# Performance work log

Measured on AMD Instinct MI355X. Metric: run time of the kernel, lower is better.

Reference implementation:

```python
import jax, jax.numpy as jnp
import numpy as np


def setup_inputs() -> dict:
    key = jax.random.key(0)
    k1, k2, k3, k4 = jax.random.split(key, 4)
    N_NODES, N_RELS, N_TRIPLES, H = 100000, 100000, 300000, 256
    node_states = jax.random.normal(k1, (N_NODES, H), dtype=jnp.float32)
    rel_states = jax.random.normal(k2, (N_RELS, H), dtype=jnp.float32)
    triples = jax.random.randint(k3, (N_TRIPLES, 3), 0, N_NODES, dtype=jnp.int64)
    # nn.Linear(2H, H): weight (H, 2H) in torch; store transposed (2H, H) for x @ W
    W = jax.random.normal(k4, (2 * H, H), dtype=jnp.float32) * (1.0 / np.sqrt(2 * H))
    b = jnp.zeros((H,), dtype=jnp.float32)
    return {"node_states": node_states, "rel_states": rel_states, "triples": triples, "W": W, "b": b}


def reference(node_states, rel_states, triples, W, b):
    # triples columns: (subj_idx, rel_idx, obj_idx)
    subj_idx, rel_idx, obj_idx = triples[:, 0], triples[:, 1], triples[:, 2]
    rel = rel_states[rel_idx]                              # (T, H)
    msg_s2o = node_states[subj_idx] + rel                  # (T, H)
    msg_o2s = node_states[obj_idx] + rel                   # (T, H)
    agg = jnp.zeros_like(node_states)
    agg = agg.at[obj_idx].add(msg_s2o)
    agg = agg.at[subj_idx].add(msg_o2s)
    h = jnp.concatenate([node_states, agg], axis=-1)       # (N, 2H)
    h = h @ W + b                                          # (N, H)
    h = jax.nn.silu(h)
    return node_states + h
```

## Files before the change

### kernel.cpp

```cpp
#include <hip/hip_runtime.h>

#define H 256
typedef unsigned int  uint;
typedef unsigned short ushort;
typedef float  floatx4 __attribute__((ext_vector_type(4)));
typedef short  shortx8 __attribute__((ext_vector_type(8)));

__device__ __forceinline__ ushort bf16rn(float f) {
    uint u = __float_as_uint(f);
    u += 0x7FFF + ((u >> 16) & 1);
    return (ushort)(u >> 16);
}
__device__ __forceinline__ uint pkbf2(float a, float b) {
    return (uint)bf16rn(a) | ((uint)bf16rn(b) << 16);
}
__device__ __forceinline__ void atomic_pk_bf16(void* addr, uint v) {
    asm volatile("global_atomic_pk_add_bf16 %0, %1, off" :: "v"(addr), "v"(v) : "memory");
}
__device__ __forceinline__ void glds16(const void* g, void* l) {
    __builtin_amdgcn_global_load_lds(
        (__attribute__((address_space(1))) void*)(unsigned long long)(g),
        (__attribute__((address_space(3))) void*)(l), 16, 0, 0);
}

__global__ __launch_bounds__(256) void wt_kernel(const float* __restrict__ W,
                                                 ushort* __restrict__ Wt) {
    int k = blockIdx.x;
    int n = threadIdx.x;
    Wt[(size_t)n * 512 + k] = bf16rn(W[(size_t)k * H + n]);
}

__global__ __launch_bounds__(256) void scatter_kernel(
    const float* __restrict__ ns, const float* __restrict__ rs,
    const int* __restrict__ trip, char* __restrict__ outbase, int n_trip)
{
    int t = blockIdx.x * 2 + (threadIdx.x >> 7);
    if (t >= n_trip) return;
    int p = threadIdx.x & 127;
    int s = trip[3 * t + 0];
    int r = trip[3 * t + 1];
    int o = trip[3 * t + 2];
    float2 vs = ((const float2*)ns)[(size_t)s * 128 + p];
    float2 vo = ((const float2*)ns)[(size_t)o * 128 + p];
    float2 vr = ((const float2*)rs)[(size_t)r * 128 + p];
    uint m_s2o = pkbf2(vs.x + vr.x, vs.y + vr.y);
    uint m_o2s = pkbf2(vo.x + vr.x, vo.y + vr.y);
    atomic_pk_bf16(outbase + (size_t)o * 1024 + p * 4, m_s2o);
    atomic_pk_bf16(outbase + (size_t)s * 1024 + p * 4, m_o2s);
}

__global__ __launch_bounds__(256) void gemm_kernel(
    const float* __restrict__ ns, const float* __restrict__ aggf,
    const ushort* __restrict__ Wt, const float* __restrict__ bias,
    float* __restrict__ out, int M)
{
    __shared__ __align__(16) ushort AsP[64 * 40];
    __shared__ __align__(16) ushort AsU[64 * 32];
    __shared__ __align__(16) ushort Bs [256 * 32];

    const int tid  = threadIdx.x;
    const int wave = tid >> 6;
    const int lane = tid & 63;
    const int fm = lane & 15, fq = lane >> 4;
    const int rowBase = blockIdx.x * 64;

    floatx4 acc[4][4] = {};

    const int am = tid >> 2, akq = tid & 3;
    int arow = rowBase + am; if (arow >= M) arow = M - 1;
    const float* aptrA = ns + (size_t)arow * H + akq * 8;
    const char*  aggp  = (const char*)aggf + (size_t)arow * 1024 + akq * 16;
    const char*  wtp   = (const char*)Wt;

#pragma unroll
    for (int kt = 0; kt < 8; ++kt) {
        __syncthreads();
        float4 v0 = *(const float4*)(aptrA + kt * 32);
        float4 v1 = *(const float4*)(aptrA + kt * 32 + 4);
#pragma unroll
        for (int j = 0; j < 4; ++j)
            glds16(wtp + (size_t)(j * 64 + am) * 1024 + kt * 64 + akq * 16,
                   &Bs[j * 2048 + tid * 8]);
        uint4 pk;
        pk.x = pkbf2(v0.x, v0.y); pk.y = pkbf2(v0.z, v0.w);
        pk.z = pkbf2(v1.x, v1.y); pk.w = pkbf2(v1.z, v1.w);
        *(uint4*)&AsP[am * 40 + akq * 8] = pk;
        __syncthreads();

        shortx8 aF[4], bF[4];
#pragma unroll
        for (int mi = 0; mi < 4; ++mi)
            aF[mi] = *(const shortx8*)&AsP[(mi * 16 + fm) * 40 + fq * 8];
#pragma unroll
        for (int ni = 0; ni < 4; ++ni)
            bF[ni] = *(const shortx8*)&Bs[(wave * 64 + ni * 16 + fm) * 32 + fq * 8];
#pragma unroll
        for (int mi = 0; mi < 4; ++mi)
#pragma unroll
            for (int ni = 0; ni < 4; ++ni)
                acc[mi][ni] = __builtin_amdgcn_mfma_f32_16x16x32_bf16(
                    aF[mi], bF[ni], acc[mi][ni], 0, 0, 0);
    }

#pragma unroll
    for (int kt = 0; kt < 8; ++kt) {
        __syncthreads();
        glds16(aggp + kt * 64, &AsU[tid * 8]);
#pragma unroll
        for (int j = 0; j < 4; ++j)
            glds16(wtp + (size_t)(j * 64 + am) * 1024 + (kt + 8) * 64 + akq * 16,
                   &Bs[j * 2048 + tid * 8]);
        __syncthreads();

        shortx8 aF[4], bF[4];
#pragma unroll
        for (int mi = 0; mi < 4; ++mi)
            aF[mi] = *(const shortx8*)&AsU[(mi * 16 + fm) * 32 + fq * 8];
#pragma unroll
        for (int ni = 0; ni < 4; ++ni)
            bF[ni] = *(const shortx8*)&Bs[(wave * 64 + ni * 16 + fm) * 32 + fq * 8];
#pragma unroll
        for (int mi = 0; mi < 4; ++mi)
#pragma unroll
            for (int ni = 0; ni < 4; ++ni)
                acc[mi][ni] = __builtin_amdgcn_mfma_f32_16x16x32_bf16(
                    aF[mi], bF[ni], acc[mi][ni], 0, 0, 0);
    }

#pragma unroll
    for (int mi = 0; mi < 4; ++mi) {
#pragma unroll
        for (int ni = 0; ni < 4; ++ni) {
            int col = wave * 64 + ni * 16 + fm;
            float bc = bias[col];
#pragma unroll
            for (int r = 0; r < 4; ++r) {
                int row = rowBase + mi * 16 + fq * 4 + r;
                if (row < M) {
                    float x = acc[mi][ni][r] + bc;
                    float sg = 1.f / (1.f + __expf(-x));
                    out[(size_t)row * H + col] = ns[(size_t)row * H + col] + x * sg;
                }
            }
        }
    }
}

extern "C" void kernel_launch(void* const* d_in, const int* in_sizes, int n_in,
                              void* d_out, int out_size, void* d_ws, size_t ws_size,
                              hipStream_t stream)
{
    const float* ns   = (const float*)d_in[0];
    const float* rs   = (const float*)d_in[1];
    const int*   tp   = (const int*)d_in[2];
    const float* Wm   = (const float*)d_in[3];
    const float* bias = (const float*)d_in[4];
    const int M      = in_sizes[0] / H;
    const int n_trip = in_sizes[2] / 3;
    float*  out = (float*)d_out;
    ushort* Wt  = (ushort*)d_ws;

    hipMemsetAsync(d_out, 0, (size_t)M * H * sizeof(float), stream);
    wt_kernel<<<dim3(512), dim3(256), 0, stream>>>(Wm, Wt);
    scatter_kernel<<<dim3((n_trip + 1) / 2), dim3(256), 0, stream>>>(
        ns, rs, tp, (char*)d_out, n_trip);
    gemm_kernel<<<dim3((M + 63) / 64), dim3(256), 0, stream>>>(
        ns, out, Wt, bias, out, M);
}
```

Measured before the change: 549.6 us.

## Pre-pack node states to bf16 in output buffer and unify GEMM A loads

```diff
diff --git a/kernel.cpp b/kernel.cpp
--- a/kernel.cpp
+++ b/kernel.cpp
@@ -13,6 +13,9 @@
 }
 __device__ __forceinline__ uint pkbf2(float a, float b) {
     return (uint)bf16rn(a) | ((uint)bf16rn(b) << 16);
+}
+__device__ __forceinline__ float bf2f(uint lo16) {
+    return __uint_as_float(lo16 << 16);
 }
 __device__ __forceinline__ void atomic_pk_bf16(void* addr, uint v) {
     asm volatile("global_atomic_pk_add_bf16 %0, %1, off" :: "v"(addr), "v"(v) : "memory");
@@ -30,9 +33,21 @@
     Wt[(size_t)n * 512 + k] = bf16rn(W[(size_t)k * H + n]);
 }
 
+__global__ __launch_bounds__(256) void prep_kernel(const float* __restrict__ ns,
+                                                   char* __restrict__ outbase, int M)
+{
+    int row = blockIdx.x * 2 + (threadIdx.x >> 7);
+    if (row >= M) return;
+    int t = threadIdx.x & 127;
+    float2 v = ((const float2*)ns)[(size_t)row * 128 + t];
+    uint* rp = (uint*)(outbase + (size_t)row * 1024);
+    rp[t]       = 0u;
+    rp[128 + t] = pkbf2(v.x, v.y);
+}
+
 __global__ __launch_bounds__(256) void scatter_kernel(
-    const float* __restrict__ ns, const float* __restrict__ rs,
-    const int* __restrict__ trip, char* __restrict__ outbase, int n_trip)
+    const float* __restrict__ rs, const int* __restrict__ trip,
+    char* __restrict__ outbase, int n_trip)
 {
     int t = blockIdx.x * 2 + (threadIdx.x >> 7);
     if (t >= n_trip) return;
@@ -40,23 +55,22 @@
     int s = trip[3 * t + 0];
     int r = trip[3 * t + 1];
     int o = trip[3 * t + 2];
-    float2 vs = ((const float2*)ns)[(size_t)s * 128 + p];
-    float2 vo = ((const float2*)ns)[(size_t)o * 128 + p];
+    uint bs = *(const uint*)(outbase + (size_t)s * 1024 + 512 + p * 4);
+    uint bo = *(const uint*)(outbase + (size_t)o * 1024 + 512 + p * 4);
     float2 vr = ((const float2*)rs)[(size_t)r * 128 + p];
-    uint m_s2o = pkbf2(vs.x + vr.x, vs.y + vr.y);
-    uint m_o2s = pkbf2(vo.x + vr.x, vo.y + vr.y);
+    uint m_s2o = pkbf2(bf2f(bs & 0xffffu) + vr.x, bf2f(bs >> 16) + vr.y);
+    uint m_o2s = pkbf2(bf2f(bo & 0xffffu) + vr.x, bf2f(bo >> 16) + vr.y);
     atomic_pk_bf16(outbase + (size_t)o * 1024 + p * 4, m_s2o);
     atomic_pk_bf16(outbase + (size_t)s * 1024 + p * 4, m_o2s);
 }
 
 __global__ __launch_bounds__(256) void gemm_kernel(
-    const float* __restrict__ ns, const float* __restrict__ aggf,
+    const float* __restrict__ ns, const char* __restrict__ arows,
     const ushort* __restrict__ Wt, const float* __restrict__ bias,
     float* __restrict__ out, int M)
 {
-    __shared__ __align__(16) ushort AsP[64 * 40];
-    __shared__ __align__(16) ushort AsU[64 * 32];
-    __shared__ __align__(16) ushort Bs [256 * 32];
+    __shared__ __align__(16) ushort As[64 * 32];
+    __shared__ __align__(16) ushort Bs[256 * 32];
 
     const int tid  = threadIdx.x;
     const int wave = tid >> 6;
@@ -68,54 +82,23 @@
 
     const int am = tid >> 2, akq = tid & 3;
     int arow = rowBase + am; if (arow >= M) arow = M - 1;
-    const float* aptrA = ns + (size_t)arow * H + akq * 8;
-    const char*  aggp  = (const char*)aggf + (size_t)arow * 1024 + akq * 16;
-    const char*  wtp   = (const char*)Wt;
+    const char* asrc = arows + (size_t)arow * 1024 + akq * 16;
+    const char* wtp  = (const char*)Wt;
 
 #pragma unroll
-    for (int kt = 0; kt < 8; ++kt) {
+    for (int kt = 0; kt < 16; ++kt) {
         __syncthreads();
-        float4 v0 = *(const float4*)(aptrA + kt * 32);
-        float4 v1 = *(const float4*)(aptrA + kt * 32 + 4);
+        glds16(asrc + ((512 + kt * 64) & 1023), &As[tid * 8]);
 #pragma unroll
         for (int j = 0; j < 4; ++j)
             glds16(wtp + (size_t)(j * 64 + am) * 1024 + kt * 64 + akq * 16,
-                   &Bs[j * 2048 + tid * 8]);
-        uint4 pk;
-        pk.x = pkbf2(v0.x, v0.y); pk.y = pkbf2(v0.z, v0.w);
-        pk.z = pkbf2(v1.x, v1.y); pk.w = pkbf2(v1.z, v1.w);
-        *(uint4*)&AsP[am * 40 + akq * 8] = pk;
-        __syncthreads();
-
-        shortx8 aF[4], bF[4];
-#pragma unroll
-        for (int mi = 0; mi < 4; ++mi)
-            aF[mi] = *(const shortx8*)&AsP[(mi * 16 + fm) * 40 + fq * 8];
-#pragma unroll
-        for (int ni = 0; ni < 4; ++ni)
-            bF[ni] = *(const shortx8*)&Bs[(wave * 64 + ni * 16 + fm) * 32 + fq * 8];
-#pragma unroll
-        for (int mi = 0; mi < 4; ++mi)
-#pragma unroll
-            for (int ni = 0; ni < 4; ++ni)
-                acc[mi][ni] = __builtin_amdgcn_mfma_f32_16x16x32_bf16(
-                    aF[mi], bF[ni], acc[mi][ni], 0, 0, 0);
-    }
-
-#pragma unroll
-    for (int kt = 0; kt < 8; ++kt) {
-        __syncthreads();
-        glds16(aggp + kt * 64, &AsU[tid * 8]);
-#pragma unroll
-        for (int j = 0; j < 4; ++j)
-            glds16(wtp + (size_t)(j * 64 + am) * 1024 + (kt + 8) * 64 + akq * 16,
                    &Bs[j * 2048 + tid * 8]);
         __syncthreads();
 
         shortx8 aF[4], bF[4];
 #pragma unroll
         for (int mi = 0; mi < 4; ++mi)
-            aF[mi] = *(const shortx8*)&AsU[(mi * 16 + fm) * 32 + fq * 8];
+            aF[mi] = *(const shortx8*)&As[(mi * 16 + fm) * 32 + fq * 8];
 #pragma unroll
         for (int ni = 0; ni < 4; ++ni)
             bF[ni] = *(const shortx8*)&Bs[(wave * 64 + ni * 16 + fm) * 32 + fq * 8];
@@ -160,10 +143,10 @@
     float*  out = (float*)d_out;
     ushort* Wt  = (ushort*)d_ws;
 
-    hipMemsetAsync(d_out, 0, (size_t)M * H * sizeof(float), stream);
+    prep_kernel<<<dim3((M + 1) / 2), dim3(256), 0, stream>>>(ns, (char*)out, M);
     wt_kernel<<<dim3(512), dim3(256), 0, stream>>>(Wm, Wt);
     scatter_kernel<<<dim3((n_trip + 1) / 2), dim3(256), 0, stream>>>(
-        ns, rs, tp, (char*)d_out, n_trip);
+        rs, tp, (char*)out, n_trip);
     gemm_kernel<<<dim3((M + 63) / 64), dim3(256), 0, stream>>>(
-        ns, out, Wt, bias, out, M);
+        ns, (const char*)out, Wt, bias, out, M);
 }
```

New measurement: 600.9 us. 1.09x slower.
